# Performance work log

Hardware: AMD Instinct MI355X
Metric: run time of the kernel (lower is better)

## Reference

```python
import jax, jax.numpy as jnp
import numpy as np

D_MSA = 256
D_PAIR = 128
N_HEADS = 8
HEAD_DIM = D_MSA // N_HEADS
EPS = 1e-5


def setup_inputs() -> dict:
    key = jax.random.key(0)
    ks = jax.random.split(key, 14)
    s = 0.02
    return {
        "msa": jax.random.normal(ks[0], (1, 64, 256, D_MSA), dtype=jnp.float32),
        "pair": jax.random.normal(ks[1], (1, 256, 256, D_PAIR), dtype=jnp.float32),
        "Wq": jax.random.normal(ks[2], (D_MSA, D_MSA), dtype=jnp.float32) * s,
        "bq": jnp.zeros((D_MSA,), jnp.float32),
        "Wk": jax.random.normal(ks[3], (D_MSA, D_MSA), dtype=jnp.float32) * s,
        "bk": jnp.zeros((D_MSA,), jnp.float32),
        "Wv": jax.random.normal(ks[4], (D_MSA, D_MSA), dtype=jnp.float32) * s,
        "bv": jnp.zeros((D_MSA,), jnp.float32),
        "Wpb": jax.random.normal(ks[5], (D_PAIR, N_HEADS), dtype=jnp.float32) * s,
        "bpb": jnp.zeros((N_HEADS,), jnp.float32),
        "Wo": jax.random.normal(ks[6], (D_MSA, D_MSA), dtype=jnp.float32) * s,
        "bo": jnp.zeros((D_MSA,), jnp.float32),
        "gamma": jnp.ones((D_MSA,), jnp.float32),
        "beta": jnp.zeros((D_MSA,), jnp.float32),
    }


def reference(msa, pair, Wq, bq, Wk, bk, Wv, bv, Wpb, bpb, Wo, bo, gamma, beta):
    B, N, L, D = msa.shape
    H, Hd = N_HEADS, HEAD_DIM
    # projections -> (B, N, L, H, Hd)
    q = (msa @ Wq + bq).reshape(B, N, L, H, Hd)
    k = (msa @ Wk + bk).reshape(B, N, L, H, Hd)
    v = (msa @ Wv + bv).reshape(B, N, L, H, Hd)
    # scores: (B, N, H, L, L)
    scores = jnp.einsum('bnihd,bnjhd->bnhij', q, k) / jnp.sqrt(jnp.float32(Hd))
    # pair bias: (B, L, L, H) -> (B, H, L, L), broadcast over N
    pb = jnp.transpose(pair @ Wpb + bpb, (0, 3, 1, 2))
    scores = scores + pb[:, None]
    attn = jax.nn.softmax(scores, axis=-1)
    attn_out = jnp.einsum('bnhij,bnjhd->bnihd', attn, v).reshape(B, N, L, D)
    attn_out = attn_out @ Wo + bo
    # residual + LayerNorm
    x = msa + attn_out
    mu = jnp.mean(x, axis=-1, keepdims=True)
    var = jnp.var(x, axis=-1, keepdims=True)
    return (x - mu) * jax.lax.rsqrt(var + EPS) * gamma + beta
```

## Files before the change

kernel.cpp:

```cpp
#include <hip/hip_runtime.h>

#define NSEQ 64
#define LL   256
#define DD   256
#define HH   8
#define HDIM 32

typedef short short8  __attribute__((ext_vector_type(8)));
typedef short short4v __attribute__((ext_vector_type(4)));
typedef float float4v __attribute__((ext_vector_type(4)));

#define MFMA16(a,b,c) __builtin_amdgcn_mfma_f32_16x16x32_bf16((a),(b),(c),0,0,0)

__device__ __forceinline__ float4v zero4() {
  float4v z;
  z[0] = 0.f; z[1] = 0.f; z[2] = 0.f; z[3] = 0.f;
  return z;
}

__device__ __forceinline__ short f2b(float f) {
  unsigned u = __float_as_uint(f);
  u = (u + 0x7fffu + ((u >> 16) & 1u)) >> 16;
  return (short)u;
}

__device__ __forceinline__ short8 cvt8(const float* p) {
  float4 a = *(const float4*)p;
  float4 b = *(const float4*)(p + 4);
  short8 r;
  r[0] = f2b(a.x); r[1] = f2b(a.y); r[2] = f2b(a.z); r[3] = f2b(a.w);
  r[4] = f2b(b.x); r[5] = f2b(b.y); r[6] = f2b(b.z); r[7] = f2b(b.w);
  return r;
}

__device__ __forceinline__ void ld_lds16(const void* g, void* l) {
  __builtin_amdgcn_global_load_lds(
      (const __attribute__((address_space(1))) unsigned int*)g,
      (__attribute__((address_space(3))) unsigned int*)l, 16, 0, 0);
}
#define WAIT_VM0() __builtin_amdgcn_s_waitcnt(0x0F70)

#define WT_OFF    0
#define PB_OFF    (4*65536*2)
#define Q_OFF     (PB_OFF + 8*65536*4)
#define K_OFF     (Q_OFF  + 16384*256*2)
#define VT_OFF    (K_OFF  + 16384*256*2)
#define MSA16_OFF (VT_OFF + 16384*256*2)
#define O_OFF     MSA16_OFF

__global__ __launch_bounds__(256) void k1_prep(
    const float* __restrict__ msa,  const float* __restrict__ pair,
    const float* __restrict__ Wq,   const float* __restrict__ Wk,
    const float* __restrict__ Wv,   const float* __restrict__ Wpb,
    const float* __restrict__ bpb,  const float* __restrict__ Wo,
    char* __restrict__ ws)
{
  __shared__ short ldsWt[16 * 136];
  int bx = blockIdx.x, tid = threadIdx.x;
  if (bx < 256) {
    float* pbw = (float*)(ws + PB_OFF);
    for (int i = tid; i < 16 * 136; i += 256) ldsWt[i] = 0;
    __syncthreads();
    {
      float4 wv4 = *(const float4*)&Wpb[tid * 4];
      int kk = (tid * 4) >> 3, n0 = (tid * 4) & 7;
      ldsWt[(n0 + 0) * 136 + kk] = f2b(wv4.x);
      ldsWt[(n0 + 1) * 136 + kk] = f2b(wv4.y);
      ldsWt[(n0 + 2) * 136 + kk] = f2b(wv4.z);
      ldsWt[(n0 + 3) * 136 + kk] = f2b(wv4.w);
    }
    __syncthreads();
    int w = tid >> 6, l = tid & 63, q = l >> 4, c = l & 15;
    int base = bx * 256 + w * 64;
    float bias = bpb[c & 7];
    short8 bf[4];
#pragma unroll
    for (int ks = 0; ks < 4; ks++)
      bf[ks] = *(const short8*)&ldsWt[c * 136 + ks * 32 + q * 8];
    float4v acc[4];
#pragma unroll
    for (int mt = 0; mt < 4; mt++) acc[mt] = zero4();
#pragma unroll
    for (int ks = 0; ks < 4; ks++) {
#pragma unroll
      for (int mt = 0; mt < 4; mt++) {
        short8 af = cvt8(&pair[(base + mt * 16 + c) * 128 + ks * 32 + q * 8]);
        acc[mt] = MFMA16(af, bf[ks], acc[mt]);
      }
    }
    if (c < 8) {
#pragma unroll
      for (int mt = 0; mt < 4; mt++) {
        float4 o;
        o.x = acc[mt][0] + bias; o.y = acc[mt][1] + bias;
        o.z = acc[mt][2] + bias; o.w = acc[mt][3] + bias;
        *(float4*)&pbw[c * 65536 + base + mt * 16 + q * 4] = o;
      }
    }
  } else if (bx < 1280) {
    int b2 = bx - 256;
    int mat = b2 >> 8, r = b2 & 255;
    const float* W = (mat == 0) ? Wq : (mat == 1) ? Wk : (mat == 2) ? Wv : Wo;
    short* wt = (short*)(ws + WT_OFF) + mat * 65536;
    wt[tid * 256 + r] = f2b(W[r * 256 + tid]);
  } else {
    int b3 = bx - 1280;
    const float* src = msa + b3 * 8192;
    short* dst = (short*)(ws + MSA16_OFF) + b3 * 8192;
#pragma unroll
    for (int i = 0; i < 8; i++) {
      int idx = i * 1024 + tid * 4;
      float4 v = *(const float4*)&src[idx];
      short4v s;
      s[0] = f2b(v.x); s[1] = f2b(v.y); s[2] = f2b(v.z); s[3] = f2b(v.w);
      *(short4v*)&dst[idx] = s;
    }
  }
}

__global__ __launch_bounds__(256) void k2_qkv(
    const float* __restrict__ bq, const float* __restrict__ bk,
    const float* __restrict__ bv, char* __restrict__ ws)
{
  __shared__ __align__(16) short lsA[128 * 128];
  __shared__ __align__(16) short lsB[128 * 128];
  int bx = blockIdx.x, tid = threadIdx.x;
  int rt = bx & 127, ct = bx >> 7;
  int m = ct >> 1, cb = (ct & 1) * 128;
  int R0 = rt * 128;
  const short* msa16 = (const short*)(ws + MSA16_OFF);
  const short* wt = (const short*)(ws + WT_OFF) + m * 65536;
  int w = tid >> 6, l = tid & 63, q = l >> 4, c = l & 15;
  int WR = (w & 1) * 64, WC = (w >> 1) * 64;
  float4v acc[4][4];
#pragma unroll
  for (int mt = 0; mt < 4; mt++)
#pragma unroll
    for (int nt = 0; nt < 4; nt++) acc[mt][nt] = zero4();

#pragma unroll 1
  for (int kk = 0; kk < 2; kk++) {
    if (kk) __syncthreads();
#pragma unroll
    for (int i = 0; i < 8; i++) {
      int ci = i * 256 + tid;
      int r = ci >> 4, pos = ci & 15;
      int kc = pos ^ (r & 7);
      ld_lds16(&msa16[(R0 + r) * 256 + kk * 128 + kc * 8], &lsA[ci * 8]);
    }
#pragma unroll
    for (int i = 0; i < 8; i++) {
      int ci = i * 256 + tid;
      int r = ci >> 4, pos = ci & 15;
      int kc = pos ^ (r & 7);
      ld_lds16(&wt[(cb + r) * 256 + kk * 128 + kc * 8], &lsB[ci * 8]);
    }
    WAIT_VM0();
    __syncthreads();
#pragma unroll
    for (int ks = 0; ks < 4; ks++) {
      short8 af[4], bf[4];
#pragma unroll
      for (int mt = 0; mt < 4; mt++) {
        int r = WR + mt * 16 + c;
        int phys = (ks * 4 + q) ^ (r & 7);
        af[mt] = *(const short8*)&lsA[r * 128 + phys * 8];
      }
#pragma unroll
      for (int nt = 0; nt < 4; nt++) {
        int r = WC + nt * 16 + c;
        int phys = (ks * 4 + q) ^ (r & 7);
        bf[nt] = *(const short8*)&lsB[r * 128 + phys * 8];
      }
#pragma unroll
      for (int mt = 0; mt < 4; mt++)
#pragma unroll
        for (int nt = 0; nt < 4; nt++)
          acc[mt][nt] = MFMA16(af[mt], bf[nt], acc[mt][nt]);
    }
  }

  const float* bp = (m == 0) ? bq : (m == 1) ? bk : bv;
  if (m < 2) {
    short* dst = (short*)(ws + (m == 0 ? Q_OFF : K_OFF));
#pragma unroll
    for (int nt = 0; nt < 4; nt++) {
      int ch = cb + WC + nt * 16 + c;
      float bb = bp[ch];
#pragma unroll
      for (int mt = 0; mt < 4; mt++) {
        int row = R0 + WR + mt * 16 + q * 4;
#pragma unroll
        for (int r = 0; r < 4; r++)
          dst[(row + r) * 256 + ch] = f2b(acc[mt][nt][r] + bb);
      }
    }
  } else {
    short* vt = (short*)(ws + VT_OFF);
    int n = R0 >> 8;
#pragma unroll
    for (int nt = 0; nt < 4; nt++) {
      int ch = cb + WC + nt * 16 + c;
      float bb = bp[ch];
#pragma unroll
      for (int mt = 0; mt < 4; mt++) {
        int j0 = (R0 & 255) + WR + mt * 16 + q * 4;
        short4v s4;
#pragma unroll
        for (int r = 0; r < 4; r++) s4[r] = f2b(acc[mt][nt][r] + bb);
        *(short4v*)&vt[((n * HH + (ch >> 5)) * HDIM + (ch & 31)) * 256 + j0] = s4;
      }
    }
  }
}

__global__ __launch_bounds__(256) void k3_attn(char* __restrict__ ws)
{
  __shared__ short P[64 * 264];
  int bx = blockIdx.x, tid = threadIdx.x;
  int n = bx >> 5, h = (bx >> 2) & 7, qq = bx & 3;
  int w = tid >> 6, l = tid & 63, q = l >> 4, c = l & 15;
  const short* qs  = (const short*)(ws + Q_OFF);
  const short* kks = (const short*)(ws + K_OFF);
  const short* vt  = (const short*)(ws + VT_OFF);
  const float* pbp = (const float*)(ws + PB_OFF) + h * 65536;
  short* os = (short*)(ws + O_OFF);
  const float scale = 0.17677669529663687f;
  int i0 = qq * 64 + w * 16;
  short8 aq = *(const short8*)&qs[(n * 256 + i0 + c) * 256 + h * 32 + q * 8];
  float4v s[16];
#pragma unroll
  for (int jt = 0; jt < 16; jt++) {
    short8 bk8 = *(const short8*)&kks[(n * 256 + jt * 16 + c) * 256 + h * 32 + q * 8];
    s[jt] = MFMA16(aq, bk8, zero4());
  }
#pragma unroll
  for (int jt = 0; jt < 16; jt++) {
#pragma unroll
    for (int r = 0; r < 4; r++) {
      float pbv = pbp[(i0 + q * 4 + r) * 256 + jt * 16 + c];
      s[jt][r] = __builtin_fmaf(s[jt][r], scale, pbv);
    }
  }
  float inv[4];
#pragma unroll
  for (int r = 0; r < 4; r++) {
    float m = s[0][r];
#pragma unroll
    for (int jt = 1; jt < 16; jt++) m = fmaxf(m, s[jt][r]);
    m = fmaxf(m, __shfl_xor(m, 1, 64));
    m = fmaxf(m, __shfl_xor(m, 2, 64));
    m = fmaxf(m, __shfl_xor(m, 4, 64));
    m = fmaxf(m, __shfl_xor(m, 8, 64));
    float rs = 0.f;
#pragma unroll
    for (int jt = 0; jt < 16; jt++) {
      float p = __expf(s[jt][r] - m);
      s[jt][r] = p;
      rs += p;
    }
    rs += __shfl_xor(rs, 1, 64);
    rs += __shfl_xor(rs, 2, 64);
    rs += __shfl_xor(rs, 4, 64);
    rs += __shfl_xor(rs, 8, 64);
    inv[r] = 1.f / rs;
  }
#pragma unroll
  for (int jt = 0; jt < 16; jt++)
#pragma unroll
    for (int r = 0; r < 4; r++)
      P[(w * 16 + q * 4 + r) * 264 + jt * 16 + c] = f2b(s[jt][r]);
  float4v o0 = zero4(), o1 = zero4();
#pragma unroll
  for (int kk = 0; kk < 8; kk++) {
    short8 ap = *(const short8*)&P[(w * 16 + c) * 264 + kk * 32 + q * 8];
    short8 b0 = *(const short8*)&vt[((n * HH + h) * HDIM + c) * 256 + kk * 32 + q * 8];
    short8 b1 = *(const short8*)&vt[((n * HH + h) * HDIM + 16 + c) * 256 + kk * 32 + q * 8];
    o0 = MFMA16(ap, b0, o0);
    o1 = MFMA16(ap, b1, o1);
  }
#pragma unroll
  for (int r = 0; r < 4; r++) {
    os[(n * 256 + i0 + q * 4 + r) * 256 + h * 32 + c]      = f2b(o0[r] * inv[r]);
    os[(n * 256 + i0 + q * 4 + r) * 256 + h * 32 + 16 + c] = f2b(o1[r] * inv[r]);
  }
}

__global__ __launch_bounds__(256) void k4_out(
    const float* __restrict__ msa, const float* __restrict__ bo,
    const float* __restrict__ gamma, const float* __restrict__ beta,
    const char* __restrict__ ws, float* __restrict__ out)
{
  __shared__ __align__(16) short lsA[64 * 128];
  __shared__ __align__(16) short lsB[256 * 128];
  int bx = blockIdx.x, tid = threadIdx.x;
  int w = tid >> 6, l = tid & 63, q = l >> 4, c = l & 15;
  int R0 = bx * 64;
  const short* osrc = (const short*)(ws + O_OFF);
  const short* wto  = (const short*)(ws + WT_OFF) + 3 * 65536;
  float4v acc[16];
#pragma unroll
  for (int nt = 0; nt < 16; nt++) acc[nt] = zero4();

#pragma unroll 1
  for (int kk = 0; kk < 2; kk++) {
    if (kk) __syncthreads();
#pragma unroll
    for (int i = 0; i < 4; i++) {
      int ci = i * 256 + tid;
      int r = ci >> 4, pos = ci & 15;
      int kc = pos ^ (r & 7);
      ld_lds16(&osrc[(R0 + r) * 256 + kk * 128 + kc * 8], &lsA[ci * 8]);
    }
#pragma unroll
    for (int i = 0; i < 16; i++) {
      int ci = i * 256 + tid;
      int r = ci >> 4, pos = ci & 15;
      int kc = pos ^ (r & 7);
      ld_lds16(&wto[r * 256 + kk * 128 + kc * 8], &lsB[ci * 8]);
    }
    WAIT_VM0();
    __syncthreads();
#pragma unroll
    for (int ks = 0; ks < 4; ks++) {
      int rA = w * 16 + c;
      int physA = (ks * 4 + q) ^ (rA & 7);
      short8 af = *(const short8*)&lsA[rA * 128 + physA * 8];
#pragma unroll
      for (int nt = 0; nt < 16; nt++) {
        int r = nt * 16 + c;
        int phys = (ks * 4 + q) ^ (r & 7);
        short8 bf = *(const short8*)&lsB[r * 128 + phys * 8];
        acc[nt] = MFMA16(af, bf, acc[nt]);
      }
    }
  }

  int r0 = R0 + w * 16;
  float s1[4] = {0, 0, 0, 0}, s2[4] = {0, 0, 0, 0};
#pragma unroll
  for (int nt = 0; nt < 16; nt++) {
    float bb = bo[nt * 16 + c];
#pragma unroll
    for (int r = 0; r < 4; r++) {
      float x = acc[nt][r] + bb + msa[(r0 + q * 4 + r) * 256 + nt * 16 + c];
      acc[nt][r] = x;
      s1[r] += x;
      s2[r] = __builtin_fmaf(x, x, s2[r]);
    }
  }
  float mu[4], rsd[4];
#pragma unroll
  for (int r = 0; r < 4; r++) {
    float a = s1[r], b = s2[r];
    a += __shfl_xor(a, 1, 64); b += __shfl_xor(b, 1, 64);
    a += __shfl_xor(a, 2, 64); b += __shfl_xor(b, 2, 64);
    a += __shfl_xor(a, 4, 64); b += __shfl_xor(b, 4, 64);
    a += __shfl_xor(a, 8, 64); b += __shfl_xor(b, 8, 64);
    float m = a * (1.f / 256.f);
    float v = __builtin_fmaf(-m, m, b * (1.f / 256.f));
    mu[r] = m;
    rsd[r] = rsqrtf(v + 1e-5f);
  }
#pragma unroll
  for (int nt = 0; nt < 16; nt++) {
    float g = gamma[nt * 16 + c], bt = beta[nt * 16 + c];
#pragma unroll
    for (int r = 0; r < 4; r++)
      out[(r0 + q * 4 + r) * 256 + nt * 16 + c] =
          (acc[nt][r] - mu[r]) * rsd[r] * g + bt;
  }
}

extern "C" void kernel_launch(void* const* d_in, const int* in_sizes, int n_in,
                              void* d_out, int out_size, void* d_ws, size_t ws_size,
                              hipStream_t stream)
{
  const float* msa   = (const float*)d_in[0];
  const float* pair  = (const float*)d_in[1];
  const float* Wq    = (const float*)d_in[2];
  const float* bq    = (const float*)d_in[3];
  const float* Wk    = (const float*)d_in[4];
  const float* bk    = (const float*)d_in[5];
  const float* Wv    = (const float*)d_in[6];
  const float* bv    = (const float*)d_in[7];
  const float* Wpb   = (const float*)d_in[8];
  const float* bpb   = (const float*)d_in[9];
  const float* Wo    = (const float*)d_in[10];
  const float* bo    = (const float*)d_in[11];
  const float* gamma = (const float*)d_in[12];
  const float* beta  = (const float*)d_in[13];
  char* ws = (char*)d_ws;
  float* out = (float*)d_out;

  hipLaunchKernelGGL(k1_prep, dim3(1792), dim3(256), 0, stream,
                     msa, pair, Wq, Wk, Wv, Wpb, bpb, Wo, ws);
  hipLaunchKernelGGL(k2_qkv, dim3(768), dim3(256), 0, stream,
                     bq, bk, bv, ws);
  hipLaunchKernelGGL(k3_attn, dim3(2048), dim3(256), 0, stream, ws);
  hipLaunchKernelGGL(k4_out, dim3(256), dim3(256), 0, stream,
                     msa, bo, gamma, beta, ws, out);
}
```

Baseline: 187.5 us.

## Store pair bias as bf16 in MFMA fragment order and head-major Q/K

```diff
diff --git a/kernel.cpp b/kernel.cpp
--- a/kernel.cpp
+++ b/kernel.cpp
@@ -22,6 +22,10 @@
   unsigned u = __float_as_uint(f);
   u = (u + 0x7fffu + ((u >> 16) & 1u)) >> 16;
   return (short)u;
+}
+
+__device__ __forceinline__ float b2f(short s) {
+  return __uint_as_float(((unsigned)(unsigned short)s) << 16);
 }
 
 __device__ __forceinline__ short8 cvt8(const float* p) {
@@ -42,6 +46,7 @@
 
 #define WT_OFF    0
 #define PB_OFF    (4*65536*2)
+#define PBF_OFF   (PB_OFF + 8*65536*2)
 #define Q_OFF     (PB_OFF + 8*65536*4)
 #define K_OFF     (Q_OFF  + 16384*256*2)
 #define VT_OFF    (K_OFF  + 16384*256*2)
@@ -58,7 +63,7 @@
   __shared__ short ldsWt[16 * 136];
   int bx = blockIdx.x, tid = threadIdx.x;
   if (bx < 256) {
-    float* pbw = (float*)(ws + PB_OFF);
+    short* pb16 = (short*)(ws + PB_OFF);
     for (int i = tid; i < 16 * 136; i += 256) ldsWt[i] = 0;
     __syncthreads();
     {
@@ -91,10 +96,10 @@
     if (c < 8) {
 #pragma unroll
       for (int mt = 0; mt < 4; mt++) {
-        float4 o;
-        o.x = acc[mt][0] + bias; o.y = acc[mt][1] + bias;
-        o.z = acc[mt][2] + bias; o.w = acc[mt][3] + bias;
-        *(float4*)&pbw[c * 65536 + base + mt * 16 + q * 4] = o;
+        short4v o;
+#pragma unroll
+        for (int r = 0; r < 4; r++) o[r] = f2b(acc[mt][r] + bias);
+        *(short4v*)&pb16[c * 65536 + base + mt * 16 + q * 4] = o;
       }
     }
   } else if (bx < 1280) {
@@ -125,6 +130,31 @@
   __shared__ __align__(16) short lsA[128 * 128];
   __shared__ __align__(16) short lsB[128 * 128];
   int bx = blockIdx.x, tid = threadIdx.x;
+  if (bx >= 768) {
+    int b = bx - 768;
+    int it16 = b & 15;
+    const short* src = (const short*)(ws + PB_OFF) + (b >> 4) * 65536 + it16 * 4096;
+    short* pbf = (short*)(ws + PBF_OFF);
+    short* lt = lsA;
+#pragma unroll
+    for (int i2 = 0; i2 < 2; i2++) {
+      int idx = i2 * 2048 + tid * 8;
+      *(short8*)&lt[(idx >> 8) * 264 + (idx & 255)] = *(const short8*)&src[idx];
+    }
+    __syncthreads();
+#pragma unroll
+    for (int i2 = 0; i2 < 4; i2++) {
+      int fid = i2 * 256 + tid;
+      int jt = fid >> 6, lane = fid & 63;
+      int qp = lane >> 4, cp = lane & 15;
+      short4v v;
+#pragma unroll
+      for (int r = 0; r < 4; r++)
+        v[r] = lt[(qp * 4 + r) * 264 + jt * 16 + cp];
+      *(short4v*)&pbf[((b * 16 + jt) * 64 + lane) * 4] = v;
+    }
+    return;
+  }
   int rt = bx & 127, ct = bx >> 7;
   int m = ct >> 1, cb = (ct & 1) * 128;
   int R0 = rt * 128;
@@ -181,23 +211,24 @@
   }
 
   const float* bp = (m == 0) ? bq : (m == 1) ? bk : bv;
+  int n = R0 >> 8;
   if (m < 2) {
     short* dst = (short*)(ws + (m == 0 ? Q_OFF : K_OFF));
 #pragma unroll
     for (int nt = 0; nt < 4; nt++) {
       int ch = cb + WC + nt * 16 + c;
       float bb = bp[ch];
+      int h = ch >> 5, hd = ch & 31;
 #pragma unroll
       for (int mt = 0; mt < 4; mt++) {
-        int row = R0 + WR + mt * 16 + q * 4;
+        int i0 = (R0 & 255) + WR + mt * 16 + q * 4;
 #pragma unroll
         for (int r = 0; r < 4; r++)
-          dst[(row + r) * 256 + ch] = f2b(acc[mt][nt][r] + bb);
+          dst[((n * HH + h) * 256 + i0 + r) * HDIM + hd] = f2b(acc[mt][nt][r] + bb);
       }
     }
   } else {
     short* vt = (short*)(ws + VT_OFF);
-    int n = R0 >> 8;
 #pragma unroll
     for (int nt = 0; nt < 4; nt++) {
       int ch = cb + WC + nt * 16 + c;
@@ -218,29 +249,29 @@
 {
   __shared__ short P[64 * 264];
   int bx = blockIdx.x, tid = threadIdx.x;
-  int n = bx >> 5, h = (bx >> 2) & 7, qq = bx & 3;
+  int qq = bx >> 9, grp = bx & 511;
+  int n = grp >> 3, h = grp & 7;
   int w = tid >> 6, l = tid & 63, q = l >> 4, c = l & 15;
-  const short* qs  = (const short*)(ws + Q_OFF);
-  const short* kks = (const short*)(ws + K_OFF);
-  const short* vt  = (const short*)(ws + VT_OFF);
-  const float* pbp = (const float*)(ws + PB_OFF) + h * 65536;
+  const short* qh = (const short*)(ws + Q_OFF) + (n * HH + h) * 256 * HDIM;
+  const short* kh = (const short*)(ws + K_OFF) + (n * HH + h) * 256 * HDIM;
+  const short* vt = (const short*)(ws + VT_OFF) + (n * HH + h) * HDIM * 256;
+  const short* pbf = (const short*)(ws + PBF_OFF) + (h * 16 + qq * 4 + w) * 16 * 256;
   short* os = (short*)(ws + O_OFF);
   const float scale = 0.17677669529663687f;
   int i0 = qq * 64 + w * 16;
-  short8 aq = *(const short8*)&qs[(n * 256 + i0 + c) * 256 + h * 32 + q * 8];
+  short8 aq = *(const short8*)&qh[(i0 + c) * HDIM + q * 8];
   float4v s[16];
 #pragma unroll
   for (int jt = 0; jt < 16; jt++) {
-    short8 bk8 = *(const short8*)&kks[(n * 256 + jt * 16 + c) * 256 + h * 32 + q * 8];
+    short8 bk8 = *(const short8*)&kh[(jt * 16 + c) * HDIM + q * 8];
     s[jt] = MFMA16(aq, bk8, zero4());
   }
 #pragma unroll
   for (int jt = 0; jt < 16; jt++) {
-#pragma unroll
-    for (int r = 0; r < 4; r++) {
-      float pbv = pbp[(i0 + q * 4 + r) * 256 + jt * 16 + c];
-      s[jt][r] = __builtin_fmaf(s[jt][r], scale, pbv);
-    }
+    short4v pv = *(const short4v*)&pbf[(jt * 64 + l) * 4];
+#pragma unroll
+    for (int r = 0; r < 4; r++)
+      s[jt][r] = __builtin_fmaf(s[jt][r], scale, b2f(pv[r]));
   }
   float inv[4];
 #pragma unroll
@@ -274,8 +305,8 @@
 #pragma unroll
   for (int kk = 0; kk < 8; kk++) {
     short8 ap = *(const short8*)&P[(w * 16 + c) * 264 + kk * 32 + q * 8];
-    short8 b0 = *(const short8*)&vt[((n * HH + h) * HDIM + c) * 256 + kk * 32 + q * 8];
-    short8 b1 = *(const short8*)&vt[((n * HH + h) * HDIM + 16 + c) * 256 + kk * 32 + q * 8];
+    short8 b0 = *(const short8*)&vt[c * 256 + kk * 32 + q * 8];
+    short8 b1 = *(const short8*)&vt[(16 + c) * 256 + kk * 32 + q * 8];
     o0 = MFMA16(ap, b0, o0);
     o1 = MFMA16(ap, b1, o1);
   }
@@ -395,7 +426,7 @@
 
   hipLaunchKernelGGL(k1_prep, dim3(1792), dim3(256), 0, stream,
                      msa, pair, Wq, Wk, Wv, Wpb, bpb, Wo, ws);
-  hipLaunchKernelGGL(k2_qkv, dim3(768), dim3(256), 0, stream,
+  hipLaunchKernelGGL(k2_qkv, dim3(896), dim3(256), 0, stream,
                      bq, bk, bv, ws);
   hipLaunchKernelGGL(k3_attn, dim3(2048), dim3(256), 0, stream, ws);
   hipLaunchKernelGGL(k4_out, dim3(256), dim3(256), 0, stream,
```

After: 179.4 us. 4.3% less time.
